# Performance work log

Hardware: AMD Instinct MI355X
Metric: run time of the kernel (lower is better)

The kernel has to match this reference:

```python
import jax, jax.numpy as jnp
import numpy as np

N, XC, YC, H, W_ = 1024, 512, 256, 8, 8
HID = 512


def setup_inputs() -> dict:
    key = jax.random.key(0)
    k = jax.random.split(key, 6)
    x_samples = jax.random.normal(k[0], (N, XC, H, W_), dtype=jnp.float32)
    y_samples = jax.random.normal(k[1], (N, YC, H, W_), dtype=jnp.float32)
    # p_mu: Linear(x_dim, hidden) -> ReLU -> Linear(hidden, y_dim)
    s1 = 1.0 / np.sqrt(XC)
    s2 = 1.0 / np.sqrt(HID)
    W1 = jax.random.uniform(k[2], (XC, HID), jnp.float32, -s1, s1)
    b1 = jax.random.uniform(k[3], (HID,), jnp.float32, -s1, s1)
    W2 = jax.random.uniform(k[4], (HID, YC), jnp.float32, -s2, s2)
    b2 = jax.random.uniform(k[5], (YC,), jnp.float32, -s2, s2)
    return {"x_samples": x_samples, "y_samples": y_samples,
            "W1": W1, "b1": b1, "W2": W2, "b2": b2}


def reference(x_samples, y_samples, W1, b1, W2, b2):
    # AdaptiveAvgPool2d(1) + flatten(1) == mean over spatial dims
    x_vec = x_samples.mean(axis=(2, 3))  # (N, x_dim)
    y_vec = y_samples.mean(axis=(2, 3))  # (N, y_dim)
    # p_mu MLP
    h = jax.nn.relu(x_vec @ W1 + b1)
    mu = h @ W2 + b2  # (N, y_dim)
    # positive: -(mu_i - y_i)^2 / 2, summed over D
    positive = (-((mu - y_vec) ** 2) / 2.0).sum(axis=-1)  # (N,)
    # negative: for each i, mean_j (y_j - mu_i)^2 / 2, summed over D
    diff = y_vec[None, :, :] - mu[:, None, :]  # (N, N, D)
    negative = (-(diff ** 2).mean(axis=1) / 2.0).sum(axis=-1)  # (N,)
    return (positive - negative).mean()
```

## Files before the change

kernel.cpp:

```cpp
#include <hip/hip_runtime.h>

#define N_SAMP 1024
#define XC_DIM 512
#define YC_DIM 256
#define HID_DIM 512

__global__ __launch_bounds__(256) void pool_kernel(
    const float* __restrict__ x, const float* __restrict__ y,
    float* __restrict__ x_vec, float* __restrict__ y_vec) {
  const long e = (long)blockIdx.x * 256 + threadIdx.x;
  const long NX = (long)N_SAMP * XC_DIM;
  const float4* p;
  float* dst;
  long o;
  if (e < NX) {
    p = (const float4*)x + e * 16;
    dst = x_vec; o = e;
  } else {
    p = (const float4*)y + (e - NX) * 16;
    dst = y_vec; o = e - NX;
  }
  float4 v[16];
#pragma unroll
  for (int j = 0; j < 16; ++j) v[j] = p[j];
  float s0 = 0.f, s1 = 0.f, s2 = 0.f, s3 = 0.f;
#pragma unroll
  for (int j = 0; j < 16; j += 4) {
    s0 += (v[j + 0].x + v[j + 0].y) + (v[j + 0].z + v[j + 0].w);
    s1 += (v[j + 1].x + v[j + 1].y) + (v[j + 1].z + v[j + 1].w);
    s2 += (v[j + 2].x + v[j + 2].y) + (v[j + 2].z + v[j + 2].w);
    s3 += (v[j + 3].x + v[j + 3].y) + (v[j + 3].z + v[j + 3].w);
  }
  dst[o] = ((s0 + s1) + (s2 + s3)) * (1.0f / 64.0f);
}

#define TBK 16

__global__ __launch_bounds__(256) void gemm1_kernel(
    const float* __restrict__ A, const float* __restrict__ B,
    float* __restrict__ Hp) {
  const int K = 512, Nn = 512;
  __shared__ float As[TBK][68];
  __shared__ float Bs[TBK][68];
  const int t = threadIdx.x;
  const int bn = blockIdx.x * 64;
  const int bm = blockIdx.y * 64;
  const int ks = blockIdx.z;

  const int arow = t >> 2, acol = (t & 3) * 4;
  const int brow = t >> 4, bcol = (t & 15) * 4;
  const int row0 = (t >> 4) * 4, col0 = (t & 15) * 4;

  float acc[4][4] = {};
  const int k0 = ks * 128;

  float4 av = *(const float4*)&A[(bm + arow) * K + k0 + acol];
  float4 bv = *(const float4*)&B[(k0 + brow) * Nn + bn + bcol];

  for (int it = 0; it < 8; ++it) {
    __syncthreads();
    As[acol + 0][arow] = av.x;
    As[acol + 1][arow] = av.y;
    As[acol + 2][arow] = av.z;
    As[acol + 3][arow] = av.w;
    *(float4*)&Bs[brow][bcol] = bv;
    __syncthreads();
    if (it < 7) {
      const int k1 = k0 + (it + 1) * TBK;
      av = *(const float4*)&A[(bm + arow) * K + k1 + acol];
      bv = *(const float4*)&B[(k1 + brow) * Nn + bn + bcol];
    }
#pragma unroll
    for (int kk = 0; kk < TBK; ++kk) {
      float4 a = *(const float4*)&As[kk][row0];
      float4 b = *(const float4*)&Bs[kk][col0];
      acc[0][0] += a.x * b.x; acc[0][1] += a.x * b.y; acc[0][2] += a.x * b.z; acc[0][3] += a.x * b.w;
      acc[1][0] += a.y * b.x; acc[1][1] += a.y * b.y; acc[1][2] += a.y * b.z; acc[1][3] += a.y * b.w;
      acc[2][0] += a.z * b.x; acc[2][1] += a.z * b.y; acc[2][2] += a.z * b.z; acc[2][3] += a.z * b.w;
      acc[3][0] += a.w * b.x; acc[3][1] += a.w * b.y; acc[3][2] += a.w * b.z; acc[3][3] += a.w * b.w;
    }
  }

  float* H = Hp + (long)ks * (N_SAMP * HID_DIM);
#pragma unroll
  for (int i = 0; i < 4; ++i) {
    float4 o;
    o.x = acc[i][0]; o.y = acc[i][1]; o.z = acc[i][2]; o.w = acc[i][3];
    *(float4*)&H[(long)(bm + row0 + i) * Nn + bn + col0] = o;
  }
}

__global__ __launch_bounds__(256) void gemm2_kernel(
    const float* __restrict__ Hp, const float* __restrict__ b1,
    const float* __restrict__ B, float* __restrict__ Mup) {
  const int K = 512, Nn = 256;
  __shared__ float As[TBK][68];
  __shared__ float Bs[TBK][68];
  const int t = threadIdx.x;
  const int bn = blockIdx.x * 64;
  const int bm = blockIdx.y * 64;
  const int ks = blockIdx.z;

  const int arow = t >> 2, acol = (t & 3) * 4;
  const int brow = t >> 4, bcol = (t & 15) * 4;
  const int row0 = (t >> 4) * 4, col0 = (t & 15) * 4;
  const long HS = (long)N_SAMP * HID_DIM;

  float acc[4][4] = {};
  const int k0 = ks * 64;

  long aidx = (long)(bm + arow) * K + k0 + acol;
  float4 a0 = *(const float4*)&Hp[aidx];
  float4 a1 = *(const float4*)&Hp[aidx + HS];
  float4 a2 = *(const float4*)&Hp[aidx + 2 * HS];
  float4 a3 = *(const float4*)&Hp[aidx + 3 * HS];
  float4 bb = *(const float4*)&b1[k0 + acol];
  float4 bv = *(const float4*)&B[(k0 + brow) * Nn + bn + bcol];

  for (int it = 0; it < 4; ++it) {
    float4 av;
    av.x = fmaxf(a0.x + a1.x + a2.x + a3.x + bb.x, 0.0f);
    av.y = fmaxf(a0.y + a1.y + a2.y + a3.y + bb.y, 0.0f);
    av.z = fmaxf(a0.z + a1.z + a2.z + a3.z + bb.z, 0.0f);
    av.w = fmaxf(a0.w + a1.w + a2.w + a3.w + bb.w, 0.0f);
    __syncthreads();
    As[acol + 0][arow] = av.x;
    As[acol + 1][arow] = av.y;
    As[acol + 2][arow] = av.z;
    As[acol + 3][arow] = av.w;
    *(float4*)&Bs[brow][bcol] = bv;
    __syncthreads();
    if (it < 3) {
      const int k1 = k0 + (it + 1) * TBK;
      aidx = (long)(bm + arow) * K + k1 + acol;
      a0 = *(const float4*)&Hp[aidx];
      a1 = *(const float4*)&Hp[aidx + HS];
      a2 = *(const float4*)&Hp[aidx + 2 * HS];
      a3 = *(const float4*)&Hp[aidx + 3 * HS];
      bb = *(const float4*)&b1[k1 + acol];
      bv = *(const float4*)&B[(k1 + brow) * Nn + bn + bcol];
    }
#pragma unroll
    for (int kk = 0; kk < TBK; ++kk) {
      float4 a = *(const float4*)&As[kk][row0];
      float4 b = *(const float4*)&Bs[kk][col0];
      acc[0][0] += a.x * b.x; acc[0][1] += a.x * b.y; acc[0][2] += a.x * b.z; acc[0][3] += a.x * b.w;
      acc[1][0] += a.y * b.x; acc[1][1] += a.y * b.y; acc[1][2] += a.y * b.z; acc[1][3] += a.y * b.w;
      acc[2][0] += a.z * b.x; acc[2][1] += a.z * b.y; acc[2][2] += a.z * b.z; acc[2][3] += a.z * b.w;
      acc[3][0] += a.w * b.x; acc[3][1] += a.w * b.y; acc[3][2] += a.w * b.z; acc[3][3] += a.w * b.w;
    }
  }

  float* M = Mup + (long)ks * (N_SAMP * YC_DIM);
#pragma unroll
  for (int i = 0; i < 4; ++i) {
    float4 o;
    o.x = acc[i][0]; o.y = acc[i][1]; o.z = acc[i][2]; o.w = acc[i][3];
    *(float4*)&M[(long)(bm + row0 + i) * Nn + bn + col0] = o;
  }
}

__global__ __launch_bounds__(256) void reduce_kernel(
    const float* __restrict__ Mup, const float* __restrict__ b2,
    const float* __restrict__ yv, float* __restrict__ colsum_mu,
    float* __restrict__ colsum_y, float* __restrict__ dot_out) {
  const int d = threadIdx.x;
  const int n0 = blockIdx.x * 4;
  const long MS = (long)N_SAMP * YC_DIM;
  const float bb = b2[d];
  float cm = 0.f, cy = 0.f, dp = 0.f;
#pragma unroll
  for (int r = 0; r < 4; ++r) {
    const long idx = (long)(n0 + r) * YC_DIM + d;
    float mu = bb;
#pragma unroll
    for (int s = 0; s < 8; ++s) mu += Mup[idx + s * MS];
    const float yy = yv[idx];
    dp += mu * yy;
    cm += mu;
    cy += yy;
  }
  atomicAdd(&colsum_mu[d], cm);
  atomicAdd(&colsum_y[d], cy);
#pragma unroll
  for (int off = 1; off < 64; off <<= 1) dp += __shfl_xor(dp, off);
  if ((d & 63) == 0) atomicAdd(dot_out, dp);
}

__global__ __launch_bounds__(256) void finalize_kernel(
    const float* __restrict__ colsum_mu, const float* __restrict__ colsum_y,
    const float* __restrict__ dot_in, float* __restrict__ out) {
  __shared__ float partial[4];
  const int t = threadIdx.x;
  float v = colsum_mu[t] * colsum_y[t];
#pragma unroll
  for (int off = 1; off < 64; off <<= 1) v += __shfl_xor(v, off);
  if ((t & 63) == 0) partial[t >> 6] = v;
  __syncthreads();
  if (t == 0) {
    float tot = partial[0] + partial[1] + partial[2] + partial[3];
    out[0] = dot_in[0] * (1.0f / 1024.0f) - tot * (1.0f / (1024.0f * 1024.0f));
  }
}

extern "C" void kernel_launch(void* const* d_in, const int* in_sizes, int n_in,
                              void* d_out, int out_size, void* d_ws, size_t ws_size,
                              hipStream_t stream) {
  const float* x  = (const float*)d_in[0];
  const float* y  = (const float*)d_in[1];
  const float* W1 = (const float*)d_in[2];
  const float* b1 = (const float*)d_in[3];
  const float* W2 = (const float*)d_in[4];
  const float* b2 = (const float*)d_in[5];
  float* out = (float*)d_out;

  char* ws = (char*)d_ws;
  float* x_vec = (float*)ws;
  float* y_vec = (float*)(ws + (2lu << 20));
  float* Hp    = (float*)(ws + (4lu << 20));
  float* Mup   = (float*)(ws + (12lu << 20));
  float* accum = (float*)(ws + (20lu << 20));
  float* colsum_mu = accum;
  float* colsum_y  = accum + 256;
  float* dotp      = accum + 512;

  hipMemsetAsync(accum, 0, 513 * sizeof(float), stream);

  pool_kernel<<<3072, 256, 0, stream>>>(x, y, x_vec, y_vec);

  gemm1_kernel<<<dim3(8, 16, 4), 256, 0, stream>>>(x_vec, W1, Hp);

  gemm2_kernel<<<dim3(4, 16, 8), 256, 0, stream>>>(Hp, b1, W2, Mup);

  reduce_kernel<<<256, 256, 0, stream>>>(Mup, b2, y_vec, colsum_mu,
                                         colsum_y, dotp);

  finalize_kernel<<<1, 256, 0, stream>>>(colsum_mu, colsum_y, dotp, out);
}
```

Measured before the change: 282.0 us.

## Coalesce pooling loads, deepen gemm1 split-K, add fold kernel, coarsen reduce

```diff
diff --git a/kernel.cpp b/kernel.cpp
--- a/kernel.cpp
+++ b/kernel.cpp
@@ -8,30 +8,34 @@
 __global__ __launch_bounds__(256) void pool_kernel(
     const float* __restrict__ x, const float* __restrict__ y,
     float* __restrict__ x_vec, float* __restrict__ y_vec) {
-  const long e = (long)blockIdx.x * 256 + threadIdx.x;
-  const long NX = (long)N_SAMP * XC_DIM;
-  const float4* p;
+  __shared__ float s[256 * 17];
+  const int t = threadIdx.x;
+  const long blk = blockIdx.x;
+  const float4* src;
   float* dst;
-  long o;
-  if (e < NX) {
-    p = (const float4*)x + e * 16;
-    dst = x_vec; o = e;
+  long obase;
+  if (blk < 2048) {
+    src = (const float4*)x; dst = x_vec; obase = blk * 256;
   } else {
-    p = (const float4*)y + (e - NX) * 16;
-    dst = y_vec; o = e - NX;
-  }
+    src = (const float4*)y; dst = y_vec; obase = (blk - 2048) * 256;
+  }
+  const float4* p = src + obase * 16;
+
   float4 v[16];
 #pragma unroll
-  for (int j = 0; j < 16; ++j) v[j] = p[j];
-  float s0 = 0.f, s1 = 0.f, s2 = 0.f, s3 = 0.f;
-#pragma unroll
-  for (int j = 0; j < 16; j += 4) {
-    s0 += (v[j + 0].x + v[j + 0].y) + (v[j + 0].z + v[j + 0].w);
-    s1 += (v[j + 1].x + v[j + 1].y) + (v[j + 1].z + v[j + 1].w);
-    s2 += (v[j + 2].x + v[j + 2].y) + (v[j + 2].z + v[j + 2].w);
-    s3 += (v[j + 3].x + v[j + 3].y) + (v[j + 3].z + v[j + 3].w);
-  }
-  dst[o] = ((s0 + s1) + (s2 + s3)) * (1.0f / 64.0f);
+  for (int k = 0; k < 16; ++k) v[k] = p[k * 256 + t];
+#pragma unroll
+  for (int k = 0; k < 16; ++k) {
+    float sv = (v[k].x + v[k].y) + (v[k].z + v[k].w);
+    const int o = k * 16 + (t >> 4);
+    const int j = t & 15;
+    s[o * 17 + j] = sv;
+  }
+  __syncthreads();
+  float acc = 0.f;
+#pragma unroll
+  for (int j = 0; j < 16; ++j) acc += s[t * 17 + j];
+  dst[obase + t] = acc * (1.0f / 64.0f);
 }
 
 #define TBK 16
@@ -52,12 +56,12 @@
   const int row0 = (t >> 4) * 4, col0 = (t & 15) * 4;
 
   float acc[4][4] = {};
-  const int k0 = ks * 128;
+  const int k0 = ks * 64;
 
   float4 av = *(const float4*)&A[(bm + arow) * K + k0 + acol];
   float4 bv = *(const float4*)&B[(k0 + brow) * Nn + bn + bcol];
 
-  for (int it = 0; it < 8; ++it) {
+  for (int it = 0; it < 4; ++it) {
     __syncthreads();
     As[acol + 0][arow] = av.x;
     As[acol + 1][arow] = av.y;
@@ -65,7 +69,7 @@
     As[acol + 3][arow] = av.w;
     *(float4*)&Bs[brow][bcol] = bv;
     __syncthreads();
-    if (it < 7) {
+    if (it < 3) {
       const int k1 = k0 + (it + 1) * TBK;
       av = *(const float4*)&A[(bm + arow) * K + k1 + acol];
       bv = *(const float4*)&B[(k1 + brow) * Nn + bn + bcol];
@@ -90,9 +94,30 @@
   }
 }
 
+__global__ __launch_bounds__(256) void foldh_kernel(
+    const float* __restrict__ Hp, const float* __restrict__ b1,
+    float* __restrict__ h) {
+  const long i = (long)blockIdx.x * 256 + threadIdx.x;
+  const long HS4 = (long)N_SAMP * HID_DIM / 4;
+  const float4* Hp4 = (const float4*)Hp;
+  float4 a = Hp4[i];
+#pragma unroll
+  for (int s = 1; s < 8; ++s) {
+    float4 b = Hp4[i + s * HS4];
+    a.x += b.x; a.y += b.y; a.z += b.z; a.w += b.w;
+  }
+  const float4 bb = ((const float4*)b1)[i & 127];
+  float4 o;
+  o.x = fmaxf(a.x + bb.x, 0.f);
+  o.y = fmaxf(a.y + bb.y, 0.f);
+  o.z = fmaxf(a.z + bb.z, 0.f);
+  o.w = fmaxf(a.w + bb.w, 0.f);
+  ((float4*)h)[i] = o;
+}
+
 __global__ __launch_bounds__(256) void gemm2_kernel(
-    const float* __restrict__ Hp, const float* __restrict__ b1,
-    const float* __restrict__ B, float* __restrict__ Mup) {
+    const float* __restrict__ A, const float* __restrict__ B,
+    float* __restrict__ Mup) {
   const int K = 512, Nn = 256;
   __shared__ float As[TBK][68];
   __shared__ float Bs[TBK][68];
@@ -104,25 +129,14 @@
   const int arow = t >> 2, acol = (t & 3) * 4;
   const int brow = t >> 4, bcol = (t & 15) * 4;
   const int row0 = (t >> 4) * 4, col0 = (t & 15) * 4;
-  const long HS = (long)N_SAMP * HID_DIM;
 
   float acc[4][4] = {};
   const int k0 = ks * 64;
 
-  long aidx = (long)(bm + arow) * K + k0 + acol;
-  float4 a0 = *(const float4*)&Hp[aidx];
-  float4 a1 = *(const float4*)&Hp[aidx + HS];
-  float4 a2 = *(const float4*)&Hp[aidx + 2 * HS];
-  float4 a3 = *(const float4*)&Hp[aidx + 3 * HS];
-  float4 bb = *(const float4*)&b1[k0 + acol];
+  float4 av = *(const float4*)&A[(bm + arow) * K + k0 + acol];
   float4 bv = *(const float4*)&B[(k0 + brow) * Nn + bn + bcol];
 
   for (int it = 0; it < 4; ++it) {
-    float4 av;
-    av.x = fmaxf(a0.x + a1.x + a2.x + a3.x + bb.x, 0.0f);
-    av.y = fmaxf(a0.y + a1.y + a2.y + a3.y + bb.y, 0.0f);
-    av.z = fmaxf(a0.z + a1.z + a2.z + a3.z + bb.z, 0.0f);
-    av.w = fmaxf(a0.w + a1.w + a2.w + a3.w + bb.w, 0.0f);
     __syncthreads();
     As[acol + 0][arow] = av.x;
     As[acol + 1][arow] = av.y;
@@ -132,12 +146,7 @@
     __syncthreads();
     if (it < 3) {
       const int k1 = k0 + (it + 1) * TBK;
-      aidx = (long)(bm + arow) * K + k1 + acol;
-      a0 = *(const float4*)&Hp[aidx];
-      a1 = *(const float4*)&Hp[aidx + HS];
-      a2 = *(const float4*)&Hp[aidx + 2 * HS];
-      a3 = *(const float4*)&Hp[aidx + 3 * HS];
-      bb = *(const float4*)&b1[k1 + acol];
+      av = *(const float4*)&A[(bm + arow) * K + k1 + acol];
       bv = *(const float4*)&B[(k1 + brow) * Nn + bn + bcol];
     }
 #pragma unroll
@@ -165,12 +174,12 @@
     const float* __restrict__ yv, float* __restrict__ colsum_mu,
     float* __restrict__ colsum_y, float* __restrict__ dot_out) {
   const int d = threadIdx.x;
-  const int n0 = blockIdx.x * 4;
+  const int n0 = blockIdx.x * 16;
   const long MS = (long)N_SAMP * YC_DIM;
   const float bb = b2[d];
   float cm = 0.f, cy = 0.f, dp = 0.f;
-#pragma unroll
-  for (int r = 0; r < 4; ++r) {
+#pragma unroll 4
+  for (int r = 0; r < 16; ++r) {
     const long idx = (long)(n0 + r) * YC_DIM + d;
     float mu = bb;
 #pragma unroll
@@ -217,9 +226,10 @@
   char* ws = (char*)d_ws;
   float* x_vec = (float*)ws;
   float* y_vec = (float*)(ws + (2lu << 20));
-  float* Hp    = (float*)(ws + (4lu << 20));
-  float* Mup   = (float*)(ws + (12lu << 20));
-  float* accum = (float*)(ws + (20lu << 20));
+  float* h     = (float*)(ws + (3lu << 20));
+  float* Hp    = (float*)(ws + (8lu << 20));
+  float* Mup   = (float*)(ws + (24lu << 20));
+  float* accum = (float*)(ws + (32lu << 20));
   float* colsum_mu = accum;
   float* colsum_y  = accum + 256;
   float* dotp      = accum + 512;
@@ -228,12 +238,14 @@
 
   pool_kernel<<<3072, 256, 0, stream>>>(x, y, x_vec, y_vec);
 
-  gemm1_kernel<<<dim3(8, 16, 4), 256, 0, stream>>>(x_vec, W1, Hp);
-
-  gemm2_kernel<<<dim3(4, 16, 8), 256, 0, stream>>>(Hp, b1, W2, Mup);
-
-  reduce_kernel<<<256, 256, 0, stream>>>(Mup, b2, y_vec, colsum_mu,
-                                         colsum_y, dotp);
+  gemm1_kernel<<<dim3(8, 16, 8), 256, 0, stream>>>(x_vec, W1, Hp);
+
+  foldh_kernel<<<512, 256, 0, stream>>>(Hp, b1, h);
+
+  gemm2_kernel<<<dim3(4, 16, 8), 256, 0, stream>>>(h, W2, Mup);
+
+  reduce_kernel<<<64, 256, 0, stream>>>(Mup, b2, y_vec, colsum_mu,
+                                        colsum_y, dotp);
 
   finalize_kernel<<<1, 256, 0, stream>>>(colsum_mu, colsum_y, dotp, out);
 }
```

After: 276.3 us. -2.0%, faster.
